# Optimization experiments

Hardware: AMD Instinct MI355X
Metric: run time of the kernel (lower is better)

## Reference

```python
import jax, jax.numpy as jnp
import numpy as np

B, N, H = 8, 256, 128
EDGE_IN = 2 * H + 1
NODE_IN = 2 * H


def _glorot(key, shape):
    fan_in, fan_out = shape[0], shape[1]
    lim = 1.0 / np.sqrt(fan_in)
    return jax.random.uniform(key, shape, jnp.float32, -lim, lim)


def setup_inputs() -> dict:
    key = jax.random.key(0)
    ks = jax.random.split(key, 12)
    node_state = jax.random.normal(ks[0], (B, N, H), jnp.float32)
    positions = jax.random.normal(ks[1], (B, N, 3), jnp.float32)
    mask = jnp.ones((B, N), jnp.float32)
    # edge_mlp: Linear(2H+1 -> H), SiLU, Linear(H -> H)  (weights stored [in, out])
    We1 = _glorot(ks[2], (EDGE_IN, H)); be1 = _glorot(ks[3], (1, H))[0]
    We2 = _glorot(ks[4], (H, H));       be2 = _glorot(ks[5], (1, H))[0]
    # node_mlp: Linear(2H -> H), SiLU, Linear(H -> H)
    Wn1 = _glorot(ks[6], (NODE_IN, H)); bn1 = _glorot(ks[7], (1, H))[0]
    Wn2 = _glorot(ks[8], (H, H));       bn2 = _glorot(ks[9], (1, H))[0]
    return {"node_state": node_state, "positions": positions, "mask": mask,
            "We1": We1, "be1": be1, "We2": We2, "be2": be2,
            "Wn1": Wn1, "bn1": bn1, "Wn2": Wn2, "bn2": bn2}


def reference(node_state, positions, mask, We1, be1, We2, be2, Wn1, bn1, Wn2, bn2):
    b, n, h = node_state.shape
    # pairwise distances [B, N, N, 1]; safe-sqrt so grad at i==j is 0 (exact fwd)
    rel = positions[:, :, None, :] - positions[:, None, :, :]
    sq = jnp.sum(rel * rel, axis=-1, keepdims=True)
    dist = jnp.where(sq > 0, jnp.sqrt(jnp.where(sq > 0, sq, 1.0)), 0.0)
    # broadcast-concat node features for all pairs -> [B, N, N, 2H+1]
    node_i = jnp.broadcast_to(node_state[:, :, None, :], (b, n, n, h))
    node_j = jnp.broadcast_to(node_state[:, None, :, :], (b, n, n, h))
    edge_input = jnp.concatenate([node_i, node_j, dist], axis=-1)
    edge_msg = jax.nn.silu(edge_input @ We1 + be1) @ We2 + be2  # [B,N,N,H]
    # pairwise validity mask [B, N, N, 1]
    edge_mask = (mask[:, None, :] * mask[:, :, None])[..., None]
    edge_msg = edge_msg * edge_mask
    # masked mean over j
    denom = jnp.clip(jnp.sum(edge_mask, axis=2), 1.0, None)  # [B,N,1]
    aggregated = jnp.sum(edge_msg, axis=2) / denom           # [B,N,H]
    node_in = jnp.concatenate([node_state, aggregated], axis=-1)
    updated = jax.nn.silu(node_in @ Wn1 + bn1) @ Wn2 + bn2
    return node_state + updated * mask[..., None]
```

## Files before the change

kernel.cpp:

```cpp
#include <hip/hip_runtime.h>
#include <hip/hip_bf16.h>
#include <math.h>

#define B_ 8
#define N_ 256
#define H_ 128
#define NODES_ (B_ * N_)

__device__ __forceinline__ float silu_fast(float x) {
    float e = __expf(-x);
    return x * __builtin_amdgcn_rcpf(1.0f + e);
}

__device__ __forceinline__ float dot128(const float* __restrict__ Wcol,
                                        const float* __restrict__ act)
{
    float wA[8], wB[8];
    #pragma unroll
    for (int u = 0; u < 8; ++u) wA[u] = Wcol[u * H_];
    float acc0 = 0.f, acc1 = 0.f;
    #pragma unroll
    for (int k = 0; k < 128; k += 16) {
        #pragma unroll
        for (int u = 0; u < 8; ++u) wB[u] = Wcol[(k + 8 + u) * H_];
        #pragma unroll
        for (int u = 0; u < 8; u += 2) {
            acc0 = fmaf(act[k + u],     wA[u],     acc0);
            acc1 = fmaf(act[k + u + 1], wA[u + 1], acc1);
        }
        if (k + 16 < 128) {
            #pragma unroll
            for (int u = 0; u < 8; ++u) wA[u] = Wcol[(k + 16 + u) * H_];
        }
        #pragma unroll
        for (int u = 0; u < 8; u += 2) {
            acc0 = fmaf(act[k + 8 + u],     wB[u],     acc0);
            acc1 = fmaf(act[k + 8 + u + 1], wB[u + 1], acc1);
        }
    }
    return acc0 + acc1;
}

__global__ __launch_bounds__(256) void k1(
    const float* __restrict__ node, const float* __restrict__ We1,
    const float* __restrict__ be1, const float* __restrict__ Wn1,
    const float* __restrict__ bn1,
    float* __restrict__ P, float* __restrict__ Q, float* __restrict__ pre)
{
    __shared__ float act[8][128];
    const int t = threadIdx.x;
    const int g = blockIdx.x >> 8;
    const int node0 = (blockIdx.x & 255) * 8;
    {
        int idx = t * 4;
        int r = idx >> 7, col = idx & 127;
        *(float4*)(&act[r][col]) = *(const float4*)(node + (size_t)(node0 + r) * H_ + col);
    }
    const float* W; const float* bias; float* op;
    if (g == 0)      { W = We1;             bias = be1;     op = P;   }
    else if (g == 1) { W = We1 + 128 * H_;  bias = nullptr; op = Q;   }
    else             { W = Wn1;             bias = bn1;     op = pre; }
    const int n  = t >> 5;
    const int c0 = (t & 31) * 4;
    const float* Wc = W + c0;
    __syncthreads();

    float4 wA[4], wB[4];
    #pragma unroll
    for (int u = 0; u < 4; ++u) wA[u] = *(const float4*)(Wc + u * H_);
    float4 a = {0.f, 0.f, 0.f, 0.f}, b = {0.f, 0.f, 0.f, 0.f};
    #pragma unroll
    for (int k = 0; k < 128; k += 8) {
        #pragma unroll
        for (int u = 0; u < 4; ++u) wB[u] = *(const float4*)(Wc + (k + 4 + u) * H_);
        #pragma unroll
        for (int u = 0; u < 4; u += 2) {
            float v0 = act[n][k + u], v1 = act[n][k + u + 1];
            a.x = fmaf(v0, wA[u].x, a.x);     a.y = fmaf(v0, wA[u].y, a.y);
            a.z = fmaf(v0, wA[u].z, a.z);     a.w = fmaf(v0, wA[u].w, a.w);
            b.x = fmaf(v1, wA[u+1].x, b.x);   b.y = fmaf(v1, wA[u+1].y, b.y);
            b.z = fmaf(v1, wA[u+1].z, b.z);   b.w = fmaf(v1, wA[u+1].w, b.w);
        }
        if (k + 8 < 128) {
            #pragma unroll
            for (int u = 0; u < 4; ++u) wA[u] = *(const float4*)(Wc + (k + 8 + u) * H_);
        }
        #pragma unroll
        for (int u = 0; u < 4; u += 2) {
            float v0 = act[n][k + 4 + u], v1 = act[n][k + 4 + u + 1];
            a.x = fmaf(v0, wB[u].x, a.x);     a.y = fmaf(v0, wB[u].y, a.y);
            a.z = fmaf(v0, wB[u].z, a.z);     a.w = fmaf(v0, wB[u].w, a.w);
            b.x = fmaf(v1, wB[u+1].x, b.x);   b.y = fmaf(v1, wB[u+1].y, b.y);
            b.z = fmaf(v1, wB[u+1].z, b.z);   b.w = fmaf(v1, wB[u+1].w, b.w);
        }
    }
    float4 r; r.x = a.x + b.x; r.y = a.y + b.y; r.z = a.z + b.z; r.w = a.w + b.w;
    if (bias) {
        float4 bv = *(const float4*)(bias + c0);
        r.x += bv.x; r.y += bv.y; r.z += bv.z; r.w += bv.w;
    }
    *(float4*)(op + (size_t)(node0 + n) * H_ + c0) = r;
}

__global__ __launch_bounds__(512) void k2(
    const float* __restrict__ P, const float* __restrict__ Q,
    const float* __restrict__ We1, const float* __restrict__ positions,
    const float* __restrict__ mask, float* __restrict__ S)
{
    __shared__ float dls[256][4];
    __shared__ float mls[256];
    __shared__ float part[4][4][128];
    const int t  = threadIdx.x;
    const int b  = blockIdx.x >> 6;
    const int i0 = (blockIdx.x & 63) * 4;

    if (t < 256) mls[t] = mask[b * N_ + t];
    {
        const int t2 = t & 255;
        const int half = t >> 8;
        const int il = t2 & 3;
        const int jb = t2 >> 2;
        const float* pb = positions + b * N_ * 3;
        const float pix = pb[(i0 + il) * 3 + 0];
        const float piy = pb[(i0 + il) * 3 + 1];
        const float piz = pb[(i0 + il) * 3 + 2];
        #pragma unroll
        for (int s = 0; s < 2; ++s) {
            int j = jb + 64 * (half * 2 + s);
            float dx = pix - pb[j * 3 + 0];
            float dy = piy - pb[j * 3 + 1];
            float dz = piz - pb[j * 3 + 2];
            float sq = dx * dx + dy * dy + dz * dz;
            dls[j][il] = (sq > 0.f) ? sqrtf(sq) : 0.f;
        }
    }
    __syncthreads();
    const int c  = t & 127;
    const int jq = t >> 7;
    const float wdc   = We1[256 * H_ + c];
    const float base0 = P[(size_t)(b * N_ + i0 + 0) * H_ + c];
    const float base1 = P[(size_t)(b * N_ + i0 + 1) * H_ + c];
    const float base2 = P[(size_t)(b * N_ + i0 + 2) * H_ + c];
    const float base3 = P[(size_t)(b * N_ + i0 + 3) * H_ + c];
    float acc0 = 0.f, acc1 = 0.f, acc2 = 0.f, acc3 = 0.f;
    const float* __restrict__ Qb = Q + (size_t)(b * N_ + jq * 64) * H_ + c;

    float qA[8], qB[8];
    #pragma unroll
    for (int u = 0; u < 8; ++u) qA[u] = Qb[u * H_];

    #pragma unroll
    for (int jj = 0; jj < 64; jj += 16) {
        #pragma unroll
        for (int u = 0; u < 8; ++u) qB[u] = Qb[(jj + 8 + u) * H_];
        #pragma unroll
        for (int u = 0; u < 8; ++u) {
            const int j = jq * 64 + jj + u;
            float mj = mls[j];
            float4 d4 = *(const float4*)(&dls[j][0]);
            float x0 = fmaf(d4.x, wdc, base0 + qA[u]);
            float x1 = fmaf(d4.y, wdc, base1 + qA[u]);
            float x2 = fmaf(d4.z, wdc, base2 + qA[u]);
            float x3 = fmaf(d4.w, wdc, base3 + qA[u]);
            acc0 = fmaf(silu_fast(x0), mj, acc0);
            acc1 = fmaf(silu_fast(x1), mj, acc1);
            acc2 = fmaf(silu_fast(x2), mj, acc2);
            acc3 = fmaf(silu_fast(x3), mj, acc3);
        }
        if (jj + 16 < 64) {
            #pragma unroll
            for (int u = 0; u < 8; ++u) qA[u] = Qb[(jj + 16 + u) * H_];
        }
        #pragma unroll
        for (int u = 0; u < 8; ++u) {
            const int j = jq * 64 + jj + 8 + u;
            float mj = mls[j];
            float4 d4 = *(const float4*)(&dls[j][0]);
            float x0 = fmaf(d4.x, wdc, base0 + qB[u]);
            float x1 = fmaf(d4.y, wdc, base1 + qB[u]);
            float x2 = fmaf(d4.z, wdc, base2 + qB[u]);
            float x3 = fmaf(d4.w, wdc, base3 + qB[u]);
            acc0 = fmaf(silu_fast(x0), mj, acc0);
            acc1 = fmaf(silu_fast(x1), mj, acc1);
            acc2 = fmaf(silu_fast(x2), mj, acc2);
            acc3 = fmaf(silu_fast(x3), mj, acc3);
        }
    }
    part[jq][0][c] = acc0; part[jq][1][c] = acc1;
    part[jq][2][c] = acc2; part[jq][3][c] = acc3;
    __syncthreads();
    {
        const int il = t >> 7;
        const int cc = t & 127;
        S[(size_t)(b * N_ + i0 + il) * H_ + cc] =
            (part[0][il][cc] + part[1][il][cc]) + (part[2][il][cc] + part[3][il][cc]);
    }
}

__global__ __launch_bounds__(256) void k3(
    const float* __restrict__ S, const float* __restrict__ pre,
    const float* __restrict__ node, const float* __restrict__ mask,
    const float* __restrict__ We2, const float* __restrict__ be2,
    const float* __restrict__ Wn1, const float* __restrict__ Wn2,
    const float* __restrict__ bn2, float* __restrict__ out)
{
    __shared__ float Sls[2][128], als[2][128], hls[2][128], nls[2][128];
    __shared__ float cs[4];
    const int t  = threadIdx.x;
    const int nb = blockIdx.x * 2;
    const int b  = nb >> 8;
    const int n  = t >> 7;
    const int c  = t & 127;

    Sls[n][c] = S[(size_t)(nb + n) * H_ + c];
    nls[n][c] = node[(size_t)(nb + n) * H_ + c];
    float mv = mask[b * N_ + t];
    #pragma unroll
    for (int off = 32; off >= 1; off >>= 1) mv += __shfl_down(mv, off);
    if ((t & 63) == 0) cs[t >> 6] = mv;
    __syncthreads();
    const float cnt = (cs[0] + cs[1]) + (cs[2] + cs[3]);
    const float mi  = mask[b * N_ + (nb & 255) + n];
    const float inv = mi * __builtin_amdgcn_rcpf(fmaxf(mi * cnt, 1.0f));

    float acc = dot128(We2 + c, &Sls[n][0]);
    als[n][c] = inv * fmaf(cnt, be2[c], acc);
    __syncthreads();

    acc = dot128(Wn1 + 128 * H_ + c, &als[n][0]);
    hls[n][c] = silu_fast(pre[(size_t)(nb + n) * H_ + c] + acc);
    __syncthreads();

    acc = dot128(Wn2 + c, &hls[n][0]);
    out[(size_t)(nb + n) * H_ + c] = nls[n][c] + mi * (acc + bn2[c]);
}

extern "C" void kernel_launch(void* const* d_in, const int* in_sizes, int n_in,
                              void* d_out, int out_size, void* d_ws, size_t ws_size,
                              hipStream_t stream)
{
    const float* node      = (const float*)d_in[0];
    const float* positions = (const float*)d_in[1];
    const float* mask      = (const float*)d_in[2];
    const float* We1       = (const float*)d_in[3];
    const float* be1       = (const float*)d_in[4];
    const float* We2       = (const float*)d_in[5];
    const float* be2       = (const float*)d_in[6];
    const float* Wn1       = (const float*)d_in[7];
    const float* bn1       = (const float*)d_in[8];
    const float* Wn2       = (const float*)d_in[9];
    const float* bn2       = (const float*)d_in[10];
    float* out = (float*)d_out;

    const size_t SZ = (size_t)NODES_ * H_;
    float* P   = (float*)d_ws;
    float* Q   = P + SZ;
    float* pre = Q + SZ;
    float* S   = pre + SZ;

    k1<<<768,  256, 0, stream>>>(node, We1, be1, Wn1, bn1, P, Q, pre);
    k2<<<512,  512, 0, stream>>>(P, Q, We1, positions, mask, S);
    k3<<<1024, 256, 0, stream>>>(S, pre, node, mask, We2, be2, Wn1, Wn2, bn2, out);
}
```

Before: 120.2 us.

## Fold We2 into Wn1, encode mask as large negative offset, split node MLP

Precomputes the product of We2 and the aggregated half of Wn1 (plus the folded be2 bias) in a small kernel, so the node stage runs one fewer 128x128 matmul per node. The j-mask is moved into Q as a -1e30 offset so SiLU goes to zero, which removes the per-pair mask multiply. The i-mask and count normalisation now happen in k2. The pair loop is rewritten with 2-wide vector FMAs to encourage packed math. The old three-matmul k3 is replaced by two float4-per-thread kernels (kB, kC), and k1 moves to 128-thread blocks. This adds two launches and relies on the large-offset trick staying numerically safe inside __expf.

```diff
diff --git a/kernel.cpp b/kernel.cpp
--- a/kernel.cpp
+++ b/kernel.cpp
@@ -7,99 +7,126 @@
 #define H_ 128
 #define NODES_ (B_ * N_)
 
+typedef float vf2 __attribute__((ext_vector_type(2)));
+
 __device__ __forceinline__ float silu_fast(float x) {
     float e = __expf(-x);
     return x * __builtin_amdgcn_rcpf(1.0f + e);
 }
 
-__device__ __forceinline__ float dot128(const float* __restrict__ Wcol,
-                                        const float* __restrict__ act)
-{
-    float wA[8], wB[8];
-    #pragma unroll
-    for (int u = 0; u < 8; ++u) wA[u] = Wcol[u * H_];
-    float acc0 = 0.f, acc1 = 0.f;
+__device__ __forceinline__ float4 colgemm128(const float* __restrict__ Wc,
+                                             const float* __restrict__ arow)
+{
+    float4 wA[8], wB[8];
+    #pragma unroll
+    for (int u = 0; u < 8; ++u) wA[u] = *(const float4*)(Wc + u * H_);
+    float4 a = {0.f,0.f,0.f,0.f}, b = {0.f,0.f,0.f,0.f};
     #pragma unroll
     for (int k = 0; k < 128; k += 16) {
         #pragma unroll
-        for (int u = 0; u < 8; ++u) wB[u] = Wcol[(k + 8 + u) * H_];
+        for (int u = 0; u < 8; ++u) wB[u] = *(const float4*)(Wc + (k + 8 + u) * H_);
         #pragma unroll
         for (int u = 0; u < 8; u += 2) {
-            acc0 = fmaf(act[k + u],     wA[u],     acc0);
-            acc1 = fmaf(act[k + u + 1], wA[u + 1], acc1);
+            float v0 = arow[k + u], v1 = arow[k + u + 1];
+            a.x = fmaf(v0, wA[u].x, a.x);   a.y = fmaf(v0, wA[u].y, a.y);
+            a.z = fmaf(v0, wA[u].z, a.z);   a.w = fmaf(v0, wA[u].w, a.w);
+            b.x = fmaf(v1, wA[u+1].x, b.x); b.y = fmaf(v1, wA[u+1].y, b.y);
+            b.z = fmaf(v1, wA[u+1].z, b.z); b.w = fmaf(v1, wA[u+1].w, b.w);
         }
         if (k + 16 < 128) {
             #pragma unroll
-            for (int u = 0; u < 8; ++u) wA[u] = Wcol[(k + 16 + u) * H_];
+            for (int u = 0; u < 8; ++u) wA[u] = *(const float4*)(Wc + (k + 16 + u) * H_);
         }
         #pragma unroll
         for (int u = 0; u < 8; u += 2) {
-            acc0 = fmaf(act[k + 8 + u],     wB[u],     acc0);
-            acc1 = fmaf(act[k + 8 + u + 1], wB[u + 1], acc1);
-        }
-    }
-    return acc0 + acc1;
-}
-
-__global__ __launch_bounds__(256) void k1(
+            float v0 = arow[k + 8 + u], v1 = arow[k + 8 + u + 1];
+            a.x = fmaf(v0, wB[u].x, a.x);   a.y = fmaf(v0, wB[u].y, a.y);
+            a.z = fmaf(v0, wB[u].z, a.z);   a.w = fmaf(v0, wB[u].w, a.w);
+            b.x = fmaf(v1, wB[u+1].x, b.x); b.y = fmaf(v1, wB[u+1].y, b.y);
+            b.z = fmaf(v1, wB[u+1].z, b.z); b.w = fmaf(v1, wB[u+1].w, b.w);
+        }
+    }
+    float4 r; r.x = a.x + b.x; r.y = a.y + b.y; r.z = a.z + b.z; r.w = a.w + b.w;
+    return r;
+}
+
+__device__ __forceinline__ float colgemm128_s(const float* __restrict__ Wc,
+                                              const float* __restrict__ arow)
+{
+    float wA[8], wB[8];
+    #pragma unroll
+    for (int u = 0; u < 8; ++u) wA[u] = Wc[u * H_];
+    float a = 0.f, b = 0.f;
+    #pragma unroll
+    for (int k = 0; k < 128; k += 16) {
+        #pragma unroll
+        for (int u = 0; u < 8; ++u) wB[u] = Wc[(k + 8 + u) * H_];
+        #pragma unroll
+        for (int u = 0; u < 8; u += 2) {
+            a = fmaf(arow[k + u],     wA[u],     a);
+            b = fmaf(arow[k + u + 1], wA[u + 1], b);
+        }
+        if (k + 16 < 128) {
+            #pragma unroll
+            for (int u = 0; u < 8; ++u) wA[u] = Wc[(k + 16 + u) * H_];
+        }
+        #pragma unroll
+        for (int u = 0; u < 8; u += 2) {
+            a = fmaf(arow[k + 8 + u],     wB[u],     a);
+            b = fmaf(arow[k + 8 + u + 1], wB[u + 1], b);
+        }
+    }
+    return a + b;
+}
+
+__global__ __launch_bounds__(128) void k0_fold(
+    const float* __restrict__ We2, const float* __restrict__ be2,
+    const float* __restrict__ Wn1, float* __restrict__ Wp, float* __restrict__ bp)
+{
+    __shared__ float arow[128];
+    const int t = threadIdx.x;
+    const int r = blockIdx.x;
+    arow[t] = (r < 128) ? We2[r * H_ + t] : be2[t];
+    __syncthreads();
+    float acc = colgemm128_s(Wn1 + 128 * H_ + t, arow);
+    if (r < 128) Wp[r * H_ + t] = acc;
+    else         bp[t] = acc;
+}
+
+__global__ __launch_bounds__(128, 3) void k1(
     const float* __restrict__ node, const float* __restrict__ We1,
     const float* __restrict__ be1, const float* __restrict__ Wn1,
-    const float* __restrict__ bn1,
+    const float* __restrict__ bn1, const float* __restrict__ mask,
     float* __restrict__ P, float* __restrict__ Q, float* __restrict__ pre)
 {
-    __shared__ float act[8][128];
+    __shared__ float act[4][128];
     const int t = threadIdx.x;
-    const int g = blockIdx.x >> 8;
-    const int node0 = (blockIdx.x & 255) * 8;
-    {
-        int idx = t * 4;
-        int r = idx >> 7, col = idx & 127;
+    const int g = blockIdx.x >> 9;
+    const int node0 = (blockIdx.x & 511) * 4;
+    {
+        int r = t >> 5, col = (t * 4) & 127;
         *(float4*)(&act[r][col]) = *(const float4*)(node + (size_t)(node0 + r) * H_ + col);
     }
-    const float* W; const float* bias; float* op;
-    if (g == 0)      { W = We1;             bias = be1;     op = P;   }
-    else if (g == 1) { W = We1 + 128 * H_;  bias = nullptr; op = Q;   }
-    else             { W = Wn1;             bias = bn1;     op = pre; }
+    const float* W; float* op;
+    if (g == 0)      { W = We1;            op = P;   }
+    else if (g == 1) { W = We1 + 128 * H_; op = Q;   }
+    else             { W = Wn1;            op = pre; }
     const int n  = t >> 5;
     const int c0 = (t & 31) * 4;
-    const float* Wc = W + c0;
-    __syncthreads();
-
-    float4 wA[4], wB[4];
-    #pragma unroll
-    for (int u = 0; u < 4; ++u) wA[u] = *(const float4*)(Wc + u * H_);
-    float4 a = {0.f, 0.f, 0.f, 0.f}, b = {0.f, 0.f, 0.f, 0.f};
-    #pragma unroll
-    for (int k = 0; k < 128; k += 8) {
-        #pragma unroll
-        for (int u = 0; u < 4; ++u) wB[u] = *(const float4*)(Wc + (k + 4 + u) * H_);
-        #pragma unroll
-        for (int u = 0; u < 4; u += 2) {
-            float v0 = act[n][k + u], v1 = act[n][k + u + 1];
-            a.x = fmaf(v0, wA[u].x, a.x);     a.y = fmaf(v0, wA[u].y, a.y);
-            a.z = fmaf(v0, wA[u].z, a.z);     a.w = fmaf(v0, wA[u].w, a.w);
-            b.x = fmaf(v1, wA[u+1].x, b.x);   b.y = fmaf(v1, wA[u+1].y, b.y);
-            b.z = fmaf(v1, wA[u+1].z, b.z);   b.w = fmaf(v1, wA[u+1].w, b.w);
-        }
-        if (k + 8 < 128) {
-            #pragma unroll
-            for (int u = 0; u < 4; ++u) wA[u] = *(const float4*)(Wc + (k + 8 + u) * H_);
-        }
-        #pragma unroll
-        for (int u = 0; u < 4; u += 2) {
-            float v0 = act[n][k + 4 + u], v1 = act[n][k + 4 + u + 1];
-            a.x = fmaf(v0, wB[u].x, a.x);     a.y = fmaf(v0, wB[u].y, a.y);
-            a.z = fmaf(v0, wB[u].z, a.z);     a.w = fmaf(v0, wB[u].w, a.w);
-            b.x = fmaf(v1, wB[u+1].x, b.x);   b.y = fmaf(v1, wB[u+1].y, b.y);
-            b.z = fmaf(v1, wB[u+1].z, b.z);   b.w = fmaf(v1, wB[u+1].w, b.w);
-        }
-    }
-    float4 r; r.x = a.x + b.x; r.y = a.y + b.y; r.z = a.z + b.z; r.w = a.w + b.w;
-    if (bias) {
-        float4 bv = *(const float4*)(bias + c0);
-        r.x += bv.x; r.y += bv.y; r.z += bv.z; r.w += bv.w;
-    }
-    *(float4*)(op + (size_t)(node0 + n) * H_ + c0) = r;
+    __syncthreads();
+
+    float4 r4 = colgemm128(W + c0, &act[n][0]);
+    if (g == 0) {
+        float4 bv = *(const float4*)(be1 + c0);
+        r4.x += bv.x; r4.y += bv.y; r4.z += bv.z; r4.w += bv.w;
+    } else if (g == 1) {
+        float off = (mask[node0 + n] - 1.0f) * 1e30f;
+        r4.x += off; r4.y += off; r4.z += off; r4.w += off;
+    } else {
+        float4 bv = *(const float4*)(bn1 + c0);
+        r4.x += bv.x; r4.y += bv.y; r4.z += bv.z; r4.w += bv.w;
+    }
+    *(float4*)(op + (size_t)(node0 + n) * H_ + c0) = r4;
 }
 
 __global__ __launch_bounds__(512) void k2(
@@ -108,13 +135,12 @@
     const float* __restrict__ mask, float* __restrict__ S)
 {
     __shared__ float dls[256][4];
-    __shared__ float mls[256];
     __shared__ float part[4][4][128];
+    __shared__ float cs;
     const int t  = threadIdx.x;
     const int b  = blockIdx.x >> 6;
     const int i0 = (blockIdx.x & 63) * 4;
 
-    if (t < 256) mls[t] = mask[b * N_ + t];
     {
         const int t2 = t & 255;
         const int half = t >> 8;
@@ -137,12 +163,13 @@
     __syncthreads();
     const int c  = t & 127;
     const int jq = t >> 7;
-    const float wdc   = We1[256 * H_ + c];
-    const float base0 = P[(size_t)(b * N_ + i0 + 0) * H_ + c];
-    const float base1 = P[(size_t)(b * N_ + i0 + 1) * H_ + c];
-    const float base2 = P[(size_t)(b * N_ + i0 + 2) * H_ + c];
-    const float base3 = P[(size_t)(b * N_ + i0 + 3) * H_ + c];
-    float acc0 = 0.f, acc1 = 0.f, acc2 = 0.f, acc3 = 0.f;
+    const float wdc = We1[256 * H_ + c];
+    const vf2 wd2 = {wdc, wdc};
+    const vf2 b01 = {P[(size_t)(b * N_ + i0 + 0) * H_ + c],
+                     P[(size_t)(b * N_ + i0 + 1) * H_ + c]};
+    const vf2 b23 = {P[(size_t)(b * N_ + i0 + 2) * H_ + c],
+                     P[(size_t)(b * N_ + i0 + 3) * H_ + c]};
+    vf2 acc01 = {0.f, 0.f}, acc23 = {0.f, 0.f};
     const float* __restrict__ Qb = Q + (size_t)(b * N_ + jq * 64) * H_ + c;
 
     float qA[8], qB[8];
@@ -156,16 +183,18 @@
         #pragma unroll
         for (int u = 0; u < 8; ++u) {
             const int j = jq * 64 + jj + u;
-            float mj = mls[j];
             float4 d4 = *(const float4*)(&dls[j][0]);
-            float x0 = fmaf(d4.x, wdc, base0 + qA[u]);
-            float x1 = fmaf(d4.y, wdc, base1 + qA[u]);
-            float x2 = fmaf(d4.z, wdc, base2 + qA[u]);
-            float x3 = fmaf(d4.w, wdc, base3 + qA[u]);
-            acc0 = fmaf(silu_fast(x0), mj, acc0);
-            acc1 = fmaf(silu_fast(x1), mj, acc1);
-            acc2 = fmaf(silu_fast(x2), mj, acc2);
-            acc3 = fmaf(silu_fast(x3), mj, acc3);
+            vf2 q2 = {qA[u], qA[u]};
+            vf2 d01 = {d4.x, d4.y}, d23 = {d4.z, d4.w};
+            vf2 x01 = __builtin_elementwise_fma(d01, wd2, b01 + q2);
+            vf2 x23 = __builtin_elementwise_fma(d23, wd2, b23 + q2);
+            vf2 e01 = {__expf(-x01.x), __expf(-x01.y)};
+            vf2 e23 = {__expf(-x23.x), __expf(-x23.y)};
+            vf2 den01 = e01 + 1.0f, den23 = e23 + 1.0f;
+            vf2 r01 = {__builtin_amdgcn_rcpf(den01.x), __builtin_amdgcn_rcpf(den01.y)};
+            vf2 r23 = {__builtin_amdgcn_rcpf(den23.x), __builtin_amdgcn_rcpf(den23.y)};
+            acc01 = __builtin_elementwise_fma(x01, r01, acc01);
+            acc23 = __builtin_elementwise_fma(x23, r23, acc23);
         }
         if (jj + 16 < 64) {
             #pragma unroll
@@ -174,65 +203,92 @@
         #pragma unroll
         for (int u = 0; u < 8; ++u) {
             const int j = jq * 64 + jj + 8 + u;
-            float mj = mls[j];
             float4 d4 = *(const float4*)(&dls[j][0]);
-            float x0 = fmaf(d4.x, wdc, base0 + qB[u]);
-            float x1 = fmaf(d4.y, wdc, base1 + qB[u]);
-            float x2 = fmaf(d4.z, wdc, base2 + qB[u]);
-            float x3 = fmaf(d4.w, wdc, base3 + qB[u]);
-            acc0 = fmaf(silu_fast(x0), mj, acc0);
-            acc1 = fmaf(silu_fast(x1), mj, acc1);
-            acc2 = fmaf(silu_fast(x2), mj, acc2);
-            acc3 = fmaf(silu_fast(x3), mj, acc3);
-        }
-    }
-    part[jq][0][c] = acc0; part[jq][1][c] = acc1;
-    part[jq][2][c] = acc2; part[jq][3][c] = acc3;
-    __syncthreads();
-    {
+            vf2 q2 = {qB[u], qB[u]};
+            vf2 d01 = {d4.x, d4.y}, d23 = {d4.z, d4.w};
+            vf2 x01 = __builtin_elementwise_fma(d01, wd2, b01 + q2);
+            vf2 x23 = __builtin_elementwise_fma(d23, wd2, b23 + q2);
+            vf2 e01 = {__expf(-x01.x), __expf(-x01.y)};
+            vf2 e23 = {__expf(-x23.x), __expf(-x23.y)};
+            vf2 den01 = e01 + 1.0f, den23 = e23 + 1.0f;
+            vf2 r01 = {__builtin_amdgcn_rcpf(den01.x), __builtin_amdgcn_rcpf(den01.y)};
+            vf2 r23 = {__builtin_amdgcn_rcpf(den23.x), __builtin_amdgcn_rcpf(den23.y)};
+            acc01 = __builtin_elementwise_fma(x01, r01, acc01);
+            acc23 = __builtin_elementwise_fma(x23, r23, acc23);
+        }
+    }
+    part[jq][0][c] = acc01.x; part[jq][1][c] = acc01.y;
+    part[jq][2][c] = acc23.x; part[jq][3][c] = acc23.y;
+    if (t < 64) {
+        float mv = mask[b * N_ + t] + mask[b * N_ + 64 + t]
+                 + mask[b * N_ + 128 + t] + mask[b * N_ + 192 + t];
+        #pragma unroll
+        for (int off = 32; off >= 1; off >>= 1) mv += __shfl_down(mv, off);
+        if (t == 0) cs = mv;
+    }
+    __syncthreads();
+    {
+        const float inv_cnt = __builtin_amdgcn_rcpf(fmaxf(cs, 1.0f));
         const int il = t >> 7;
         const int cc = t & 127;
-        S[(size_t)(b * N_ + i0 + il) * H_ + cc] =
-            (part[0][il][cc] + part[1][il][cc]) + (part[2][il][cc] + part[3][il][cc]);
-    }
-}
-
-__global__ __launch_bounds__(256) void k3(
+        const float mi = mask[b * N_ + i0 + il];
+        S[(size_t)(b * N_ + i0 + il) * H_ + cc] = (mi * inv_cnt) *
+            ((part[0][il][cc] + part[1][il][cc]) + (part[2][il][cc] + part[3][il][cc]));
+    }
+}
+
+__global__ __launch_bounds__(128, 3) void kB(
     const float* __restrict__ S, const float* __restrict__ pre,
-    const float* __restrict__ node, const float* __restrict__ mask,
-    const float* __restrict__ We2, const float* __restrict__ be2,
-    const float* __restrict__ Wn1, const float* __restrict__ Wn2,
-    const float* __restrict__ bn2, float* __restrict__ out)
-{
-    __shared__ float Sls[2][128], als[2][128], hls[2][128], nls[2][128];
-    __shared__ float cs[4];
-    const int t  = threadIdx.x;
-    const int nb = blockIdx.x * 2;
-    const int b  = nb >> 8;
-    const int n  = t >> 7;
-    const int c  = t & 127;
-
-    Sls[n][c] = S[(size_t)(nb + n) * H_ + c];
-    nls[n][c] = node[(size_t)(nb + n) * H_ + c];
-    float mv = mask[b * N_ + t];
-    #pragma unroll
-    for (int off = 32; off >= 1; off >>= 1) mv += __shfl_down(mv, off);
-    if ((t & 63) == 0) cs[t >> 6] = mv;
-    __syncthreads();
-    const float cnt = (cs[0] + cs[1]) + (cs[2] + cs[3]);
-    const float mi  = mask[b * N_ + (nb & 255) + n];
-    const float inv = mi * __builtin_amdgcn_rcpf(fmaxf(mi * cnt, 1.0f));
-
-    float acc = dot128(We2 + c, &Sls[n][0]);
-    als[n][c] = inv * fmaf(cnt, be2[c], acc);
-    __syncthreads();
-
-    acc = dot128(Wn1 + 128 * H_ + c, &als[n][0]);
-    hls[n][c] = silu_fast(pre[(size_t)(nb + n) * H_ + c] + acc);
-    __syncthreads();
-
-    acc = dot128(Wn2 + c, &hls[n][0]);
-    out[(size_t)(nb + n) * H_ + c] = nls[n][c] + mi * (acc + bn2[c]);
+    const float* __restrict__ Wp, const float* __restrict__ bp,
+    const float* __restrict__ mask, float* __restrict__ hidden)
+{
+    __shared__ float act[4][128];
+    const int t = threadIdx.x;
+    const int node0 = blockIdx.x * 4;
+    {
+        int r = t >> 5, col = (t * 4) & 127;
+        *(float4*)(&act[r][col]) = *(const float4*)(S + (size_t)(node0 + r) * H_ + col);
+    }
+    const int n  = t >> 5;
+    const int c0 = (t & 31) * 4;
+    __syncthreads();
+    float4 a = colgemm128(Wp + c0, &act[n][0]);
+    const float mi = mask[node0 + n];
+    float4 p4 = *(const float4*)(pre + (size_t)(node0 + n) * H_ + c0);
+    float4 bv = *(const float4*)(bp + c0);
+    float4 h;
+    h.x = silu_fast(p4.x + a.x + mi * bv.x);
+    h.y = silu_fast(p4.y + a.y + mi * bv.y);
+    h.z = silu_fast(p4.z + a.z + mi * bv.z);
+    h.w = silu_fast(p4.w + a.w + mi * bv.w);
+    *(float4*)(hidden + (size_t)(node0 + n) * H_ + c0) = h;
+}
+
+__global__ __launch_bounds__(128, 3) void kC(
+    const float* __restrict__ hidden, const float* __restrict__ node,
+    const float* __restrict__ Wn2, const float* __restrict__ bn2,
+    const float* __restrict__ mask, float* __restrict__ out)
+{
+    __shared__ float act[4][128];
+    const int t = threadIdx.x;
+    const int node0 = blockIdx.x * 4;
+    {
+        int r = t >> 5, col = (t * 4) & 127;
+        *(float4*)(&act[r][col]) = *(const float4*)(hidden + (size_t)(node0 + r) * H_ + col);
+    }
+    const int n  = t >> 5;
+    const int c0 = (t & 31) * 4;
+    __syncthreads();
+    float4 a = colgemm128(Wn2 + c0, &act[n][0]);
+    const float mi = mask[node0 + n];
+    float4 n4 = *(const float4*)(node + (size_t)(node0 + n) * H_ + c0);
+    float4 bv = *(const float4*)(bn2 + c0);
+    float4 r4;
+    r4.x = n4.x + mi * (a.x + bv.x);
+    r4.y = n4.y + mi * (a.y + bv.y);
+    r4.z = n4.z + mi * (a.z + bv.z);
+    r4.w = n4.w + mi * (a.w + bv.w);
+    *(float4*)(out + (size_t)(node0 + n) * H_ + c0) = r4;
 }
 
 extern "C" void kernel_launch(void* const* d_in, const int* in_sizes, int n_in,
@@ -253,12 +309,17 @@
     float* out = (float*)d_out;
 
     const size_t SZ = (size_t)NODES_ * H_;
-    float* P   = (float*)d_ws;
-    float* Q   = P + SZ;
-    float* pre = Q + SZ;
-    float* S   = pre + SZ;
-
-    k1<<<768,  256, 0, stream>>>(node, We1, be1, Wn1, bn1, P, Q, pre);
-    k2<<<512,  512, 0, stream>>>(P, Q, We1, positions, mask, S);
-    k3<<<1024, 256, 0, stream>>>(S, pre, node, mask, We2, be2, Wn1, Wn2, bn2, out);
-}
+    float* P      = (float*)d_ws;
+    float* Q      = P + SZ;
+    float* pre    = Q + SZ;
+    float* S      = pre + SZ;
+    float* Wp     = S + SZ;
+    float* bp     = Wp + H_ * H_;
+    float* hidden = P;
+
+    k0_fold<<<129,  128, 0, stream>>>(We2, be2, Wn1, Wp, bp);
+    k1     <<<1536, 128, 0, stream>>>(node, We1, be1, Wn1, bn1, mask, P, Q, pre);
+    k2     <<<512,  512, 0, stream>>>(P, Q, We1, positions, mask, S);
+    kB     <<<512,  128, 0, stream>>>(S, pre, Wp, bp, mask, hidden);
+    kC     <<<512,  128, 0, stream>>>(hidden, node, Wn2, bn2, mask, out);
+}
```

New measurement: 355.8 us. 196% more time.
